# Kernel tuning notes

Hardware: AMD Instinct MI355X
Metric: run time of the kernel (lower is better)

## Reference

```python
import jax, jax.numpy as jnp
import numpy as np

B, N, D = 4, 2048, 512
H = 8            # num_heads (even)
HE = H // 2      # effective heads = 4
DH = D // H      # head_dim = 64
LAMBDA_INIT = 0.8
EPS = 1e-5


def setup_inputs() -> dict:
    key = jax.random.key(0)
    ks = jax.random.split(key, 10)
    return {
        "q": jax.random.normal(ks[0], (B, N, D), jnp.float32),
        "k": jax.random.normal(ks[1], (B, N, D), jnp.float32),
        "v": jax.random.normal(ks[2], (B, N, D), jnp.float32),
        "lambda_q1": 0.1 * jax.random.normal(ks[3], (DH,), jnp.float32),
        "lambda_k1": 0.1 * jax.random.normal(ks[4], (DH,), jnp.float32),
        "lambda_q2": 0.1 * jax.random.normal(ks[5], (DH,), jnp.float32),
        "lambda_k2": 0.1 * jax.random.normal(ks[6], (DH,), jnp.float32),
        "norm_w": jnp.ones((2 * DH,), jnp.float32),
        "out_w": 0.02 * jax.random.normal(ks[7], (D, D), jnp.float32),  # torch Linear weight [out,in]
        "out_b": jnp.zeros((D,), jnp.float32),
    }


def reference(q, k, v, lambda_q1, lambda_k1, lambda_q2, lambda_k2, norm_w, out_w, out_b):
    b, nq, d = q.shape
    nk = k.shape[1]
    # split heads: q,k -> [B, 2*HE, N, DH]; v -> [B, HE, Nk, 2*DH]
    qh = q.reshape(b, nq, 2 * HE, DH).transpose(0, 2, 1, 3) * (DH ** -0.5)
    kh = k.reshape(b, nk, 2 * HE, DH).transpose(0, 2, 1, 3)
    vh = v.reshape(b, nk, HE, 2 * DH).transpose(0, 2, 1, 3)
    scores = jnp.einsum('bhqd,bhkd->bhqk', qh, kh)          # [B, 2HE, Nq, Nk]
    probs = jax.nn.softmax(scores, axis=-1)
    probs = probs.reshape(b, HE, 2, nq, nk)
    lam = (jnp.exp(jnp.sum(lambda_q1 * lambda_k1))
           - jnp.exp(jnp.sum(lambda_q2 * lambda_k2)) + LAMBDA_INIT)
    diff = probs[:, :, 0] - lam * probs[:, :, 1]            # [B, HE, Nq, Nk]
    out = jnp.einsum('bhqk,bhkd->bhqd', diff, vh)           # [B, HE, Nq, 2*DH]
    # per-head RMSNorm over last dim (2*DH), elementwise affine
    out = out * jax.lax.rsqrt(jnp.mean(out * out, axis=-1, keepdims=True) + EPS)
    out = out * norm_w * (1.0 - LAMBDA_INIT)
    out = out.transpose(0, 2, 1, 3).reshape(b, nq, d)
    return out @ out_w.T + out_b
```

## Files before the change

### kernel.cpp

```cpp
#include <hip/hip_runtime.h>
#include <math.h>

#define BB 4
#define NN 2048
#define DD 512
#define LAMBDA_INIT 0.8f
#define EPSV 1e-5f

typedef __attribute__((ext_vector_type(8))) short bf16x8;
typedef __attribute__((ext_vector_type(4))) float f32x4;
typedef __attribute__((ext_vector_type(16))) float f32x16;
typedef unsigned short u16;
typedef __attribute__((ext_vector_type(4))) u16 u16x4;
typedef __attribute__((ext_vector_type(8))) u16 u16x8;
typedef __attribute__((ext_vector_type(4))) unsigned u32x4;

__device__ __forceinline__ u16 f2bf(float f) {
  unsigned u = __builtin_bit_cast(unsigned, f);
  u = (u + 0x7FFFu + ((u >> 16) & 1u)) >> 16;
  return (u16)u;
}

__device__ __forceinline__ void gload16(const void* g, void* l) {
  __builtin_amdgcn_global_load_lds((const __attribute__((address_space(1))) unsigned*)g,
                                   (__attribute__((address_space(3))) unsigned*)l, 16, 0, 0);
}

__device__ __forceinline__ f32x16 fz16() {
  f32x16 z;
  #pragma unroll
  for (int i = 0; i < 16; ++i) z[i] = 0.f;
  return z;
}

__device__ __forceinline__ void plswap(unsigned &a, unsigned &b) {
  asm("v_permlane32_swap_b32 %0, %1" : "+v"(a), "+v"(b));
}
__device__ __forceinline__ float xhalf_add(float x) {
  unsigned a = __builtin_bit_cast(unsigned, x), b;
  asm("v_mov_b32 %0, %1" : "=v"(b) : "v"(a));
  asm("v_permlane32_swap_b32 %0, %1" : "+v"(a), "+v"(b));
  return __builtin_bit_cast(float, a) + __builtin_bit_cast(float, b);
}

__global__ __launch_bounds__(256) void prep_kernel(
    const float* __restrict__ q, const float* __restrict__ k, const float* __restrict__ w,
    u16* __restrict__ Qb, u16* __restrict__ Kb, u16* __restrict__ Wb)
{
  const int t = threadIdx.x;
  const int bid = blockIdx.x;
  if (bid >= BB * NN) {
    const size_t idx = (size_t)(bid - BB * NN) * 256 + t;
    float4 f = *(const float4*)&w[idx * 4];
    u16x4 o = { f2bf(f.x), f2bf(f.y), f2bf(f.z), f2bf(f.w) };
    *(u16x4*)&Wb[idx * 4] = o;
    return;
  }
  const size_t row = bid;
  const int n = bid & (NN - 1);
  const int b = bid >> 11;
  if (t < 128) {
    const float s = 0.125f * 1.4426950408889634f;
    float4 f = *(const float4*)&q[row * DD + t * 4];
    u16x4 o = { f2bf(f.x * s), f2bf(f.y * s), f2bf(f.z * s), f2bf(f.w * s) };
    *(u16x4*)&Qb[row * DD + t * 4] = o;
  } else {
    const int f0 = (t - 128) * 4;
    float4 f = *(const float4*)&k[row * DD + f0];
    const int he = f0 >> 7, fi = f0 & 127;
    const int gi = fi >> 3, lo = fi & 7;
    const int gi2 = (gi & 8) | ((gi & 7) ^ (n & 7));
    u16x4 o = { f2bf(f.x), f2bf(f.y), f2bf(f.z), f2bf(f.w) };
    *(u16x4*)&Kb[((size_t)(b * 4 + he) * NN + n) * 128 + gi2 * 8 + lo] = o;
  }
}

__global__ __launch_bounds__(256) void v_prep_kernel(const float* __restrict__ v, u16* __restrict__ Vbt) {
  __shared__ u16 Ls[64][72];
  const int t = threadIdx.x;
  const int n0 = blockIdx.x * 64;
  const int d0 = blockIdx.y * 64;
  const int z  = blockIdx.z;
  #pragma unroll
  for (int p = 0; p < 4; ++p) {
    int n = p * 16 + (t >> 4), f4 = t & 15;
    float4 rv = *(const float4*)&v[((size_t)((z >> 2) * NN + n0 + n)) * DD + (z & 3) * 128 + d0 + f4 * 4];
    Ls[n][f4*4+0] = f2bf(rv.x); Ls[n][f4*4+1] = f2bf(rv.y);
    Ls[n][f4*4+2] = f2bf(rv.z); Ls[n][f4*4+3] = f2bf(rv.w);
  }
  __syncthreads();
  #pragma unroll
  for (int rep = 0; rep < 2; ++rep) {
    const int sid   = rep * 256 + t;
    const int tt    = sid >> 8;
    const int rem   = sid & 255;
    const int i_rel = rem >> 6;
    const int ls    = rem & 63;
    const int i_    = (d0 >> 4) + i_rel;
    const int j     = i_ * 8 + (ls >> 3);
    const int s0    = (ls & 7) ^ (j & 7);
    const int dl    = 2 * (i_rel * 8 + (ls >> 3)) + (s0 >> 2);
    const int nl0   = tt * 32 + (s0 & 3) * 8;
    u16x8 o;
    #pragma unroll
    for (int jj = 0; jj < 8; ++jj) o[jj] = Ls[nl0 + jj][dl];
    const int tile = blockIdx.x * 2 + tt;
    *(u16x8*)&Vbt[((size_t)z * 64 + tile) * 4096 + i_ * 512 + ls * 8] = o;
  }
}

#define ISSUE_K(dst, kv0) do { \
  _Pragma("unroll") for (int i_ = 0; i_ < 8; ++i_) \
    gload16(kgb + (((size_t)(kv0) + i_ * 4 + (l >> 4)) << 7) + ((l & 15) << 3), (dst) + i_ * 512); \
  __builtin_amdgcn_sched_barrier(0); } while (0)

#define ISSUE_V(dst, kv0) do { \
  _Pragma("unroll") for (int i_ = 0; i_ < 8; ++i_) \
    gload16(vgb + ((size_t)((kv0) >> 5)) * 4096 + i_ * 512 + l * 8, (dst) + i_ * 512); \
  __builtin_amdgcn_sched_barrier(0); } while (0)

#define WAIT_VM0 do { asm volatile("s_waitcnt vmcnt(0)" ::: "memory"); \
  __builtin_amdgcn_sched_barrier(0); } while (0)

__global__ __launch_bounds__(256, 2) void attn10_kernel(
    const u16* __restrict__ Qb, const u16* __restrict__ Kb, const u16* __restrict__ Vbt,
    const float* __restrict__ lq1, const float* __restrict__ lk1,
    const float* __restrict__ lq2, const float* __restrict__ lk2,
    const float* __restrict__ norm_w, u16* __restrict__ Xb)
{
  __shared__ __align__(16) u16 smem[32768];
  __shared__ float stats[2][2][2][32];

  u16* KB = smem;
  u16* VB = smem + 16384;

  const int tid = threadIdx.x;
  const int w   = tid >> 6;
  const int l   = tid & 63;
  const int hi  = l >> 5;
  const int q   = l & 31;
  const int kvh = w & 1;
  const int qh  = w >> 1;

  const int bid0 = blockIdx.x;
  const int bid = (bid0 & 7) * 64 + (bid0 >> 3);
  const int qt = bid & 31;
  const int he = (bid >> 5) & 3;
  const int b  = bid >> 7;
  const int q0 = qt * 64;
  const int bhe = b * 4 + he;
  const int qrow = q0 + qh * 32 + q;

  float lp1 = lq1[l] * lk1[l], lp2 = lq2[l] * lk2[l];
  #pragma unroll
  for (int off = 32; off; off >>= 1) { lp1 += __shfl_xor(lp1, off); lp2 += __shfl_xor(lp2, off); }
  const float lam = __expf(lp1) - __expf(lp2) + LAMBDA_INIT;
  asm volatile("" :: "v"(lam));

  bf16x8 qf[2][4];
  {
    const u16* qp = Qb + ((size_t)(b * NN) + qrow) * DD + he * 128 + hi * 8;
    #pragma unroll
    for (int h = 0; h < 2; ++h)
      #pragma unroll
      for (int dk = 0; dk < 4; ++dk)
        qf[h][dk] = *(const bf16x8*)(qp + h * 64 + dk * 16);
  }
  WAIT_VM0;
  #pragma unroll
  for (int h = 0; h < 2; ++h)
    #pragma unroll
    for (int dk = 0; dk < 4; ++dk)
      asm volatile("" :: "v"(qf[h][dk]));

  const u16* kgb = Kb + (size_t)bhe * NN * 128;
  const u16* vgb = Vbt + (size_t)bhe * 64 * 4096;
  const int kvb = kvh * 1024;

  if (qh == 0) ISSUE_K(&KB[kvh * 8192], kvb);
  else         ISSUE_V(&VB[kvh * 8192], kvb);

  f32x16 O[2][4];
  #pragma unroll
  for (int h = 0; h < 2; ++h)
    #pragma unroll
    for (int dt = 0; dt < 4; ++dt) O[h][dt] = fz16();
  float sl[2] = {0.f, 0.f};

  const int jq  = (q >> 1) & 7;
  const int dq1 = (q & 1) << 2;

  for (int tt = 0; tt < 32; ++tt) {
    WAIT_VM0;
    __builtin_amdgcn_s_barrier();
    __builtin_amdgcn_sched_barrier(0);

    if (tt != 31) {
      const int kvn = kvb + (tt + 1) * 32;
      const int db = (tt + 1) & 1;
      if (qh == 0) ISSUE_K(&KB[(kvh * 2 + db) * 4096], kvn);
      else         ISSUE_V(&VB[(kvh * 2 + db) * 4096], kvn);
    }

    const u16* Kcur = &KB[(kvh * 2 + (tt & 1)) * 4096];
    const u16* Vcur = &VB[(kvh * 2 + (tt & 1)) * 4096];

    f32x16 S[2];
    __builtin_amdgcn_s_setprio(1);
    #pragma unroll
    for (int h = 0; h < 2; ++h) {
      f32x16 acc = fz16();
      #pragma unroll
      for (int dk = 0; dk < 4; ++dk) {
        const int gd = h * 8 + dk * 2 + hi;
        const int g2 = (gd & 8) | ((gd & 7) ^ (q & 7));
        bf16x8 kf = *(const bf16x8*)&Kcur[q * 128 + g2 * 8];
        acc = __builtin_amdgcn_mfma_f32_32x32x16_bf16(kf, qf[h][dk], acc, 0, 0, 0);
      }
      S[h] = acc;
    }
    __builtin_amdgcn_s_setprio(0);

    bf16x8 pb[2][2];
    #pragma unroll
    for (int h = 0; h < 2; ++h) {
      #pragma unroll
      for (int r = 0; r < 16; ++r)
        S[h][r] = __builtin_amdgcn_exp2f(S[h][r]);
      float y0 = (S[h][0]  + S[h][1])  + (S[h][2]  + S[h][3]);
      float y1 = (S[h][4]  + S[h][5])  + (S[h][6]  + S[h][7]);
      float y2 = (S[h][8]  + S[h][9])  + (S[h][10] + S[h][11]);
      float y3 = (S[h][12] + S[h][13]) + (S[h][14] + S[h][15]);
      sl[h] += (y0 + y1) + (y2 + y3);

      unsigned PK[8];
      #pragma unroll
      for (int p2 = 0; p2 < 8; ++p2)
        asm("v_cvt_pk_bf16_f32 %0, %1, %2" : "=v"(PK[p2]) : "v"(S[h][2*p2]), "v"(S[h][2*p2+1]));
      #pragma unroll
      for (int kb = 0; kb < 2; ++kb) {
        unsigned w0 = PK[4*kb + 0], w2v = PK[4*kb + 2];
        unsigned w1 = PK[4*kb + 1], w3v = PK[4*kb + 3];
        plswap(w0, w2v);
        plswap(w1, w3v);
        union { u32x4 u; bf16x8 v; } cv;
        cv.u = (u32x4){ w0, w1, w2v, w3v };
        pb[h][kb] = cv.v;
      }
    }

    __builtin_amdgcn_s_setprio(1);
    #pragma unroll
    for (int kk = 0; kk < 2; ++kk)
      #pragma unroll
      for (int dt = 0; dt < 4; ++dt) {
        const int j = dt * 16 + (q >> 1);
        const int s8 = (dq1 + kk * 2 + hi) ^ jq;
        bf16x8 vf = *(const bf16x8*)&Vcur[j * 64 + s8 * 8];
        O[0][dt] = __builtin_amdgcn_mfma_f32_32x32x16_bf16(vf, pb[0][kk], O[0][dt], 0, 0, 0);
        O[1][dt] = __builtin_amdgcn_mfma_f32_32x32x16_bf16(vf, pb[1][kk], O[1][dt], 0, 0, 0);
      }
    __builtin_amdgcn_s_setprio(0);
  }

  const float slr0 = xhalf_add(sl[0]);
  const float slr1 = xhalf_add(sl[1]);
  __syncthreads();
  if (hi == 0) {
    stats[qh][kvh][0][q] = slr0;
    stats[qh][kvh][1][q] = slr1;
  }
  __syncthreads();
  float L[2];
  #pragma unroll
  for (int h = 0; h < 2; ++h)
    L[h] = stats[qh][0][h][q] + stats[qh][1][h][q];

  float* xch = (float*)smem;
  __syncthreads();
  if (kvh == 1) {
    #pragma unroll
    for (int h = 0; h < 2; ++h)
      #pragma unroll
      for (int dt = 0; dt < 4; ++dt)
        #pragma unroll
        for (int r = 0; r < 16; ++r)
          xch[qh * 8192 + ((h * 4 + dt) * 16 + r) * 64 + l] = O[h][dt][r];
  }
  __syncthreads();
  if (kvh == 0) {
    #pragma unroll
    for (int h = 0; h < 2; ++h)
      #pragma unroll
      for (int dt = 0; dt < 4; ++dt)
        #pragma unroll
        for (int r = 0; r < 16; ++r)
          O[h][dt][r] += xch[qh * 8192 + ((h * 4 + dt) * 16 + r) * 64 + l];

    const float i1 = 1.f / L[0];
    const float i2 = lam / L[1];
    float ss = 0.f;
    f32x16 od[4];
    #pragma unroll
    for (int dt = 0; dt < 4; ++dt)
      #pragma unroll
      for (int r = 0; r < 16; ++r) {
        float o = O[0][dt][r] * i1 - O[1][dt][r] * i2;
        od[dt][r] = o; ss += o * o;
      }
    ss += __shfl_xor(ss, 32);
    const float rstd = rsqrtf(ss * (1.f / 128.f) + EPSV);
    const size_t xo = ((size_t)(b * NN) + qrow) * DD + he * 128;
    #pragma unroll
    for (int dt = 0; dt < 4; ++dt)
      #pragma unroll
      for (int rq = 0; rq < 4; ++rq) {
        const int d0 = dt * 32 + rq * 8 + hi * 4;
        const float4 nw = *(const float4*)&norm_w[d0];
        u16x4 ov;
        ov[0] = f2bf(od[dt][rq*4 + 0] * rstd * nw.x * 0.2f);
        ov[1] = f2bf(od[dt][rq*4 + 1] * rstd * nw.y * 0.2f);
        ov[2] = f2bf(od[dt][rq*4 + 2] * rstd * nw.z * 0.2f);
        ov[3] = f2bf(od[dt][rq*4 + 3] * rstd * nw.w * 0.2f);
        *(u16x4*)&Xb[xo + d0] = ov;
      }
  }
}

#define PLOAD(k0) do { \
    _Pragma("unroll") for (int p_ = 0; p_ < 2; ++p_) { \
      int idx_ = p_*256 + t; int r_ = idx_ >> 3, gi_ = idx_ & 7; \
      ra[p_] = *(const u16x8*)&Xb[(size_t)(row0 + r_) * DD + (k0) + gi_*8]; \
      rb[p_] = *(const u16x8*)&Wb[(size_t)(col0 + r_) * DD + (k0) + gi_*8]; } \
  } while (0)
#define PWRITE(bi) do { \
    _Pragma("unroll") for (int p_ = 0; p_ < 2; ++p_) { \
      int idx_ = p_*256 + t; int r_ = idx_ >> 3, gi_ = idx_ & 7; \
      *(u16x8*)&As[bi][r_*64 + ((gi_ ^ (r_ & 7)) << 3)] = ra[p_]; \
      *(u16x8*)&Bs[bi][r_*64 + ((gi_ ^ (r_ & 7)) << 3)] = rb[p_]; } \
  } while (0)

__global__ __launch_bounds__(256, 2) void proj_mfma_kernel(
    const u16* __restrict__ Xb, const u16* __restrict__ Wb,
    const float* __restrict__ bias, float* __restrict__ out)
{
  __shared__ __align__(16) u16 As[2][64*64];
  __shared__ __align__(16) u16 Bs[2][64*64];
  const int t = threadIdx.x;
  const int w = t >> 6, l = t & 63, g = l >> 4, c = l & 15;
  const int wm = w >> 1, wn = w & 1;
  const int row0 = blockIdx.x * 64, col0 = blockIdx.y * 64;

  u16x8 ra[2], rb[2];
  f32x4 acc[2][2];
  #pragma unroll
  for (int i = 0; i < 2; ++i)
    #pragma unroll
    for (int j = 0; j < 2; ++j) acc[i][j] = (f32x4){0,0,0,0};
  float bj[2];
  #pragma unroll
  for (int j = 0; j < 2; ++j) bj[j] = bias[col0 + wn*32 + j*16 + c];

  PLOAD(0);
  PWRITE(0);
  __syncthreads();
  for (int s = 0; s < 8; ++s) {
    const int bi = s & 1;
    if (s < 7) PLOAD((s + 1) * 64);
    #pragma unroll
    for (int kc = 0; kc < 2; ++kc) {
      bf16x8 af[2], bfv[2];
      #pragma unroll
      for (int i = 0; i < 2; ++i) {
        int rowa = wm*32 + i*16 + c;
        af[i]  = *(const bf16x8*)&As[bi][rowa*64 + (((kc*4 + g) ^ (c & 7)) << 3)];
        int rowb = wn*32 + i*16 + c;
        bfv[i] = *(const bf16x8*)&Bs[bi][rowb*64 + (((kc*4 + g) ^ (c & 7)) << 3)];
      }
      #pragma unroll
      for (int i = 0; i < 2; ++i)
        #pragma unroll
        for (int j = 0; j < 2; ++j)
          acc[i][j] = __builtin_amdgcn_mfma_f32_16x16x32_bf16(af[i], bfv[j], acc[i][j], 0, 0, 0);
    }
    if (s < 7) PWRITE((s + 1) & 1);
    __syncthreads();
  }
  #pragma unroll
  for (int i = 0; i < 2; ++i)
    #pragma unroll
    for (int j = 0; j < 2; ++j)
      #pragma unroll
      for (int rr = 0; rr < 4; ++rr)
        out[(size_t)(row0 + wm*32 + i*16 + g*4 + rr) * DD + col0 + wn*32 + j*16 + c] = acc[i][j][rr] + bj[j];
}

extern "C" void kernel_launch(void* const* d_in, const int* in_sizes, int n_in,
                              void* d_out, int out_size, void* d_ws, size_t ws_size,
                              hipStream_t stream) {
    const float* q      = (const float*)d_in[0];
    const float* k      = (const float*)d_in[1];
    const float* v      = (const float*)d_in[2];
    const float* lq1    = (const float*)d_in[3];
    const float* lk1    = (const float*)d_in[4];
    const float* lq2    = (const float*)d_in[5];
    const float* lk2    = (const float*)d_in[6];
    const float* norm_w = (const float*)d_in[7];
    const float* out_w  = (const float*)d_in[8];
    const float* out_b  = (const float*)d_in[9];
    float* out = (float*)d_out;

    u16* Qb  = (u16*)d_ws;
    u16* Kb  = (u16*)((char*)d_ws + (8u  << 20));
    u16* Vbt = (u16*)((char*)d_ws + (16u << 20));
    u16* Wb  = (u16*)((char*)d_ws + (24u << 20));
    u16* Xb  = (u16*)((char*)d_ws + (25u << 20));

    prep_kernel<<<BB * NN + 256, 256, 0, stream>>>(q, k, out_w, Qb, Kb, Wb);
    v_prep_kernel<<<dim3(32, 2, 16), 256, 0, stream>>>(v, Vbt);
    attn10_kernel<<<512, 256, 0, stream>>>(Qb, Kb, Vbt, lq1, lk1, lq2, lk2, norm_w, Xb);
    proj_mfma_kernel<<<dim3(128, 8), 256, 0, stream>>>(Xb, Wb, out_b, out);
}
```

Measured before the change: 89.00 us.

## Double query tile per block and triple-buffer K/V loads with deeper prefetch

The attention kernel now runs 512 threads per block, each covering 128 query rows, so one K/V tile in LDS serves twice as many queries. All eight waves split the K and V global-to-LDS loads, and a three-stage ring buffer prefetches two tiles ahead, waiting only for the oldest batch via a partial vmcnt wait. This is meant to halve K/V reload traffic per query and hide load latency better. In exchange it uses more LDS and a larger block, which can lower occupancy, and the cross-wave reduction of partial outputs is serialized over two passes.

```diff
diff --git a/kernel.cpp b/kernel.cpp
--- a/kernel.cpp
+++ b/kernel.cpp
@@ -109,30 +109,29 @@
   }
 }
 
-#define ISSUE_K(dst, kv0) do { \
-  _Pragma("unroll") for (int i_ = 0; i_ < 8; ++i_) \
-    gload16(kgb + (((size_t)(kv0) + i_ * 4 + (l >> 4)) << 7) + ((l & 15) << 3), (dst) + i_ * 512); \
+#define ISSUE_K4(dst, kv0, half) do { \
+  _Pragma("unroll") for (int i_ = 0; i_ < 4; ++i_) { int ii_ = (half)*4 + i_; \
+    gload16(kgb + (((size_t)(kv0) + ii_ * 4 + (l >> 4)) << 7) + ((l & 15) << 3), (dst) + ii_ * 512); } \
   __builtin_amdgcn_sched_barrier(0); } while (0)
 
-#define ISSUE_V(dst, kv0) do { \
-  _Pragma("unroll") for (int i_ = 0; i_ < 8; ++i_) \
-    gload16(vgb + ((size_t)((kv0) >> 5)) * 4096 + i_ * 512 + l * 8, (dst) + i_ * 512); \
+#define ISSUE_V4(dst, kv0, half) do { \
+  _Pragma("unroll") for (int i_ = 0; i_ < 4; ++i_) { int ii_ = (half)*4 + i_; \
+    gload16(vgb + ((size_t)((kv0) >> 5)) * 4096 + ii_ * 512 + l * 8, (dst) + ii_ * 512); } \
   __builtin_amdgcn_sched_barrier(0); } while (0)
 
+#define WAIT_VM(n) do { asm volatile("s_waitcnt vmcnt(" #n ")" ::: "memory"); \
+  __builtin_amdgcn_sched_barrier(0); } while (0)
 #define WAIT_VM0 do { asm volatile("s_waitcnt vmcnt(0)" ::: "memory"); \
   __builtin_amdgcn_sched_barrier(0); } while (0)
 
-__global__ __launch_bounds__(256, 2) void attn10_kernel(
+__global__ __launch_bounds__(512, 2) void attn11_kernel(
     const u16* __restrict__ Qb, const u16* __restrict__ Kb, const u16* __restrict__ Vbt,
     const float* __restrict__ lq1, const float* __restrict__ lk1,
     const float* __restrict__ lq2, const float* __restrict__ lk2,
     const float* __restrict__ norm_w, u16* __restrict__ Xb)
 {
-  __shared__ __align__(16) u16 smem[32768];
-  __shared__ float stats[2][2][2][32];
-
-  u16* KB = smem;
-  u16* VB = smem + 16384;
+  __shared__ __align__(16) u16 smem[49152];
+  __shared__ float stats[4][2][2][32];
 
   const int tid = threadIdx.x;
   const int w   = tid >> 6;
@@ -142,12 +141,18 @@
   const int kvh = w & 1;
   const int qh  = w >> 1;
 
+  const bool jK   = w < 4;
+  const int  jrem = jK ? w : (w - 4);
+  const int  jkvh = jrem >> 1;
+  const int  jhalf= jrem & 1;
+  const int  jkvb = jkvh * 1024;
+
   const int bid0 = blockIdx.x;
-  const int bid = (bid0 & 7) * 64 + (bid0 >> 3);
-  const int qt = bid & 31;
-  const int he = (bid >> 5) & 3;
-  const int b  = bid >> 7;
-  const int q0 = qt * 64;
+  const int bid = (bid0 & 7) * 32 + (bid0 >> 3);
+  const int qt = bid & 15;
+  const int he = (bid >> 4) & 3;
+  const int b  = bid >> 6;
+  const int q0 = qt * 128;
   const int bhe = b * 4 + he;
   const int qrow = q0 + qh * 32 + q;
 
@@ -175,10 +180,13 @@
 
   const u16* kgb = Kb + (size_t)bhe * NN * 128;
   const u16* vgb = Vbt + (size_t)bhe * 64 * 4096;
-  const int kvb = kvh * 1024;
-
-  if (qh == 0) ISSUE_K(&KB[kvh * 8192], kvb);
-  else         ISSUE_V(&VB[kvh * 8192], kvb);
+
+  #pragma unroll
+  for (int pt = 0; pt < 2; ++pt) {
+    u16* dst = (jK ? smem : smem + 24576) + (jkvh * 3 + pt) * 4096;
+    if (jK) ISSUE_K4(dst, jkvb + pt * 32, jhalf);
+    else    ISSUE_V4(dst, jkvb + pt * 32, jhalf);
+  }
 
   f32x16 O[2][4];
   #pragma unroll
@@ -190,20 +198,21 @@
   const int jq  = (q >> 1) & 7;
   const int dq1 = (q & 1) << 2;
 
+  int scur = 0, spre = 2;
   for (int tt = 0; tt < 32; ++tt) {
-    WAIT_VM0;
+    WAIT_VM(4);
     __builtin_amdgcn_s_barrier();
     __builtin_amdgcn_sched_barrier(0);
 
-    if (tt != 31) {
-      const int kvn = kvb + (tt + 1) * 32;
-      const int db = (tt + 1) & 1;
-      if (qh == 0) ISSUE_K(&KB[(kvh * 2 + db) * 4096], kvn);
-      else         ISSUE_V(&VB[(kvh * 2 + db) * 4096], kvn);
-    }
-
-    const u16* Kcur = &KB[(kvh * 2 + (tt & 1)) * 4096];
-    const u16* Vcur = &VB[(kvh * 2 + (tt & 1)) * 4096];
+    {
+      const int nt = (tt + 2) & 31;
+      u16* dst = (jK ? smem : smem + 24576) + (jkvh * 3 + spre) * 4096;
+      if (jK) ISSUE_K4(dst, jkvb + nt * 32, jhalf);
+      else    ISSUE_V4(dst, jkvb + nt * 32, jhalf);
+    }
+
+    const u16* Kcur = smem + (kvh * 3 + scur) * 4096;
+    const u16* Vcur = smem + 24576 + (kvh * 3 + scur) * 4096;
 
     f32x16 S[2];
     __builtin_amdgcn_s_setprio(1);
@@ -261,11 +270,16 @@
         O[1][dt] = __builtin_amdgcn_mfma_f32_32x32x16_bf16(vf, pb[1][kk], O[1][dt], 0, 0, 0);
       }
     __builtin_amdgcn_s_setprio(0);
-  }
+
+    scur = (scur == 2) ? 0 : scur + 1;
+    spre = (spre == 2) ? 0 : spre + 1;
+  }
+
+  WAIT_VM0;
+  __syncthreads();
 
   const float slr0 = xhalf_add(sl[0]);
   const float slr1 = xhalf_add(sl[1]);
-  __syncthreads();
   if (hi == 0) {
     stats[qh][kvh][0][q] = slr0;
     stats[qh][kvh][1][q] = slr1;
@@ -277,26 +291,33 @@
     L[h] = stats[qh][0][h][q] + stats[qh][1][h][q];
 
   float* xch = (float*)smem;
+  #pragma unroll
+  for (int qp = 0; qp < 2; ++qp) {
+    const bool act = (qh >> 1) == qp;
+    __syncthreads();
+    if (act && kvh == 1) {
+      #pragma unroll
+      for (int h = 0; h < 2; ++h)
+        #pragma unroll
+        for (int dt = 0; dt < 4; ++dt)
+          #pragma unroll
+          for (int r = 0; r < 16; ++r)
+            xch[(qh & 1) * 8192 + ((h * 4 + dt) * 16 + r) * 64 + l] = O[h][dt][r];
+    }
+    __syncthreads();
+    if (act && kvh == 0) {
+      #pragma unroll
+      for (int h = 0; h < 2; ++h)
+        #pragma unroll
+        for (int dt = 0; dt < 4; ++dt)
+          #pragma unroll
+          for (int r = 0; r < 16; ++r)
+            O[h][dt][r] += xch[(qh & 1) * 8192 + ((h * 4 + dt) * 16 + r) * 64 + l];
+    }
+  }
   __syncthreads();
-  if (kvh == 1) {
-    #pragma unroll
-    for (int h = 0; h < 2; ++h)
-      #pragma unroll
-      for (int dt = 0; dt < 4; ++dt)
-        #pragma unroll
-        for (int r = 0; r < 16; ++r)
-          xch[qh * 8192 + ((h * 4 + dt) * 16 + r) * 64 + l] = O[h][dt][r];
-  }
-  __syncthreads();
+
   if (kvh == 0) {
-    #pragma unroll
-    for (int h = 0; h < 2; ++h)
-      #pragma unroll
-      for (int dt = 0; dt < 4; ++dt)
-        #pragma unroll
-        for (int r = 0; r < 16; ++r)
-          O[h][dt][r] += xch[qh * 8192 + ((h * 4 + dt) * 16 + r) * 64 + l];
-
     const float i1 = 1.f / L[0];
     const float i2 = lam / L[1];
     float ss = 0.f;
@@ -418,6 +439,6 @@
 
     prep_kernel<<<BB * NN + 256, 256, 0, stream>>>(q, k, out_w, Qb, Kb, Wb);
     v_prep_kernel<<<dim3(32, 2, 16), 256, 0, stream>>>(v, Vbt);
-    attn10_kernel<<<512, 256, 0, stream>>>(Qb, Kb, Vbt, lq1, lk1, lq2, lk2, norm_w, Xb);
+    attn11_kernel<<<256, 512, 0, stream>>>(Qb, Kb, Vbt, lq1, lk1, lq2, lk2, norm_w, Xb);
     proj_mfma_kernel<<<dim3(128, 8), 256, 0, stream>>>(Xb, Wb, out_b, out);
 }
```

Result: faster. 86.87 us (-2.4%).

## Software-pipeline attention loop: overlap PV of previous tile with QK and softmax

Applied to the files above, without the earlier changes.

Restructures the attention main loop so each iteration computes QK for the current KV tile, then the PV product for the previous tile's probabilities, then the exp/pack for the current tile. MFMA work can then overlap the transcendental and pack instructions instead of running strictly one after the other. V tiles go into a triple buffer because a V tile is consumed one iteration later than its K tile, so shared memory grows and the stats array moves into that buffer. The last iteration issues a redundant wrap-around prefetch, which is waited on before smem reuse.

```diff
diff --git a/kernel.cpp b/kernel.cpp
--- a/kernel.cpp
+++ b/kernel.cpp
@@ -122,14 +122,62 @@
 #define WAIT_VM0 do { asm volatile("s_waitcnt vmcnt(0)" ::: "memory"); \
   __builtin_amdgcn_sched_barrier(0); } while (0)
 
-__global__ __launch_bounds__(256, 2) void attn10_kernel(
+#define DO_QK(Kcur, S) do { \
+  __builtin_amdgcn_s_setprio(1); \
+  _Pragma("unroll") for (int h = 0; h < 2; ++h) { \
+    f32x16 acc = fz16(); \
+    _Pragma("unroll") for (int dk = 0; dk < 4; ++dk) { \
+      const int gd = h * 8 + dk * 2 + hi; \
+      const int g2 = (gd & 8) | ((gd & 7) ^ (q & 7)); \
+      bf16x8 kf = *(const bf16x8*)&(Kcur)[q * 128 + g2 * 8]; \
+      acc = __builtin_amdgcn_mfma_f32_32x32x16_bf16(kf, qf[h][dk], acc, 0, 0, 0); \
+    } \
+    S[h] = acc; \
+  } \
+  __builtin_amdgcn_s_setprio(0); } while (0)
+
+#define DO_PV(Vcur, pbX) do { \
+  __builtin_amdgcn_s_setprio(1); \
+  _Pragma("unroll") for (int kk = 0; kk < 2; ++kk) \
+    _Pragma("unroll") for (int dt = 0; dt < 4; ++dt) { \
+      const int j = dt * 16 + (q >> 1); \
+      const int s8 = (dq1 + kk * 2 + hi) ^ jq; \
+      bf16x8 vf = *(const bf16x8*)&(Vcur)[j * 64 + s8 * 8]; \
+      O[0][dt] = __builtin_amdgcn_mfma_f32_32x32x16_bf16(vf, pbX[0][kk], O[0][dt], 0, 0, 0); \
+      O[1][dt] = __builtin_amdgcn_mfma_f32_32x32x16_bf16(vf, pbX[1][kk], O[1][dt], 0, 0, 0); \
+    } \
+  __builtin_amdgcn_s_setprio(0); } while (0)
+
+#define DO_SM(S, pbX) do { \
+  _Pragma("unroll") for (int h = 0; h < 2; ++h) { \
+    _Pragma("unroll") for (int r = 0; r < 16; ++r) \
+      S[h][r] = __builtin_amdgcn_exp2f(S[h][r]); \
+    float y0 = (S[h][0]  + S[h][1])  + (S[h][2]  + S[h][3]); \
+    float y1 = (S[h][4]  + S[h][5])  + (S[h][6]  + S[h][7]); \
+    float y2 = (S[h][8]  + S[h][9])  + (S[h][10] + S[h][11]); \
+    float y3 = (S[h][12] + S[h][13]) + (S[h][14] + S[h][15]); \
+    sl[h] += (y0 + y1) + (y2 + y3); \
+    unsigned PK[8]; \
+    _Pragma("unroll") for (int p2 = 0; p2 < 8; ++p2) \
+      asm("v_cvt_pk_bf16_f32 %0, %1, %2" : "=v"(PK[p2]) : "v"(S[h][2*p2]), "v"(S[h][2*p2+1])); \
+    _Pragma("unroll") for (int kb = 0; kb < 2; ++kb) { \
+      unsigned w0 = PK[4*kb + 0], w2v = PK[4*kb + 2]; \
+      unsigned w1 = PK[4*kb + 1], w3v = PK[4*kb + 3]; \
+      plswap(w0, w2v); \
+      plswap(w1, w3v); \
+      union { u32x4 u; bf16x8 v; } cv; \
+      cv.u = (u32x4){ w0, w1, w2v, w3v }; \
+      pbX[h][kb] = cv.v; \
+    } \
+  } } while (0)
+
+__global__ __launch_bounds__(256, 2) void attn12_kernel(
     const u16* __restrict__ Qb, const u16* __restrict__ Kb, const u16* __restrict__ Vbt,
     const float* __restrict__ lq1, const float* __restrict__ lk1,
     const float* __restrict__ lq2, const float* __restrict__ lk2,
     const float* __restrict__ norm_w, u16* __restrict__ Xb)
 {
-  __shared__ __align__(16) u16 smem[32768];
-  __shared__ float stats[2][2][2][32];
+  __shared__ __align__(16) u16 smem[40960];
 
   u16* KB = smem;
   u16* VB = smem + 16384;
@@ -177,8 +225,8 @@
   const u16* vgb = Vbt + (size_t)bhe * 64 * 4096;
   const int kvb = kvh * 1024;
 
-  if (qh == 0) ISSUE_K(&KB[kvh * 8192], kvb);
-  else         ISSUE_V(&VB[kvh * 8192], kvb);
+  if (qh == 0) ISSUE_K(&KB[(kvh * 2 + 0) * 4096], kvb);
+  else         ISSUE_V(&VB[(kvh * 3 + 0) * 4096], kvb);
 
   f32x16 O[2][4];
   #pragma unroll
@@ -186,97 +234,76 @@
     #pragma unroll
     for (int dt = 0; dt < 4; ++dt) O[h][dt] = fz16();
   float sl[2] = {0.f, 0.f};
+  bf16x8 pbP[2][2];
 
   const int jq  = (q >> 1) & 7;
   const int dq1 = (q & 1) << 2;
 
-  for (int tt = 0; tt < 32; ++tt) {
+  {
     WAIT_VM0;
     __builtin_amdgcn_s_barrier();
     __builtin_amdgcn_sched_barrier(0);
-
-    if (tt != 31) {
-      const int kvn = kvb + (tt + 1) * 32;
-      const int db = (tt + 1) & 1;
-      if (qh == 0) ISSUE_K(&KB[(kvh * 2 + db) * 4096], kvn);
-      else         ISSUE_V(&VB[(kvh * 2 + db) * 4096], kvn);
+    if (qh == 0) ISSUE_K(&KB[(kvh * 2 + 1) * 4096], kvb + 32);
+    else         ISSUE_V(&VB[(kvh * 3 + 1) * 4096], kvb + 32);
+    const u16* Kcur = &KB[(kvh * 2 + 0) * 4096];
+    f32x16 S[2];
+    DO_QK(Kcur, S);
+    DO_SM(S, pbP);
+  }
+
+  int vprev = 0, vnext = 2;
+  for (int tt = 1; tt < 32; ++tt) {
+    WAIT_VM0;
+    __builtin_amdgcn_s_barrier();
+    __builtin_amdgcn_sched_barrier(0);
+
+    {
+      const int kvn = kvb + ((tt + 1) & 31) * 32;
+      if (qh == 0) ISSUE_K(&KB[(kvh * 2 + ((tt + 1) & 1)) * 4096], kvn);
+      else         ISSUE_V(&VB[(kvh * 3 + vnext) * 4096], kvn);
     }
 
-    const u16* Kcur = &KB[(kvh * 2 + (tt & 1)) * 4096];
-    const u16* Vcur = &VB[(kvh * 2 + (tt & 1)) * 4096];
+    const u16* Kcur  = &KB[(kvh * 2 + (tt & 1)) * 4096];
+    const u16* Vprev = &VB[(kvh * 3 + vprev) * 4096];
 
     f32x16 S[2];
-    __builtin_amdgcn_s_setprio(1);
-    #pragma unroll
-    for (int h = 0; h < 2; ++h) {
-      f32x16 acc = fz16();
-      #pragma unroll
-      for (int dk = 0; dk < 4; ++dk) {
-        const int gd = h * 8 + dk * 2 + hi;
-        const int g2 = (gd & 8) | ((gd & 7) ^ (q & 7));
-        bf16x8 kf = *(const bf16x8*)&Kcur[q * 128 + g2 * 8];
-        acc = __builtin_amdgcn_mfma_f32_32x32x16_bf16(kf, qf[h][dk], acc, 0, 0, 0);
-      }
-      S[h] = acc;
-    }
-    __builtin_amdgcn_s_setprio(0);
-
-    bf16x8 pb[2][2];
-    #pragma unroll
-    for (int h = 0; h < 2; ++h) {
-      #pragma unroll
-      for (int r = 0; r < 16; ++r)
-        S[h][r] = __builtin_amdgcn_exp2f(S[h][r]);
-      float y0 = (S[h][0]  + S[h][1])  + (S[h][2]  + S[h][3]);
-      float y1 = (S[h][4]  + S[h][5])  + (S[h][6]  + S[h][7]);
-      float y2 = (S[h][8]  + S[h][9])  + (S[h][10] + S[h][11]);
-      float y3 = (S[h][12] + S[h][13]) + (S[h][14] + S[h][15]);
-      sl[h] += (y0 + y1) + (y2 + y3);
-
-      unsigned PK[8];
-      #pragma unroll
-      for (int p2 = 0; p2 < 8; ++p2)
-        asm("v_cvt_pk_bf16_f32 %0, %1, %2" : "=v"(PK[p2]) : "v"(S[h][2*p2]), "v"(S[h][2*p2+1]));
-      #pragma unroll
-      for (int kb = 0; kb < 2; ++kb) {
-        unsigned w0 = PK[4*kb + 0], w2v = PK[4*kb + 2];
-        unsigned w1 = PK[4*kb + 1], w3v = PK[4*kb + 3];
-        plswap(w0, w2v);
-        plswap(w1, w3v);
-        union { u32x4 u; bf16x8 v; } cv;
-        cv.u = (u32x4){ w0, w1, w2v, w3v };
-        pb[h][kb] = cv.v;
-      }
-    }
-
-    __builtin_amdgcn_s_setprio(1);
-    #pragma unroll
-    for (int kk = 0; kk < 2; ++kk)
-      #pragma unroll
-      for (int dt = 0; dt < 4; ++dt) {
-        const int j = dt * 16 + (q >> 1);
-        const int s8 = (dq1 + kk * 2 + hi) ^ jq;
-        bf16x8 vf = *(const bf16x8*)&Vcur[j * 64 + s8 * 8];
-        O[0][dt] = __builtin_amdgcn_mfma_f32_32x32x16_bf16(vf, pb[0][kk], O[0][dt], 0, 0, 0);
-        O[1][dt] = __builtin_amdgcn_mfma_f32_32x32x16_bf16(vf, pb[1][kk], O[1][dt], 0, 0, 0);
-      }
-    __builtin_amdgcn_s_setprio(0);
-  }
+    DO_QK(Kcur, S);
+    DO_PV(Vprev, pbP);
+    bf16x8 pbN[2][2];
+    DO_SM(S, pbN);
+    #pragma unroll
+    for (int h = 0; h < 2; ++h)
+      #pragma unroll
+      for (int kb = 0; kb < 2; ++kb)
+        pbP[h][kb] = pbN[h][kb];
+
+    vprev = (vprev == 2) ? 0 : vprev + 1;
+    vnext = (vnext == 2) ? 0 : vnext + 1;
+  }
+
+  {
+    const u16* Vlast = &VB[(kvh * 3 + 1) * 4096];
+    DO_PV(Vlast, pbP);
+  }
+
+  WAIT_VM0;
+  __syncthreads();
+
+  float* xch   = (float*)smem;
+  float* stats = (float*)smem + 16384;
 
   const float slr0 = xhalf_add(sl[0]);
   const float slr1 = xhalf_add(sl[1]);
-  __syncthreads();
   if (hi == 0) {
-    stats[qh][kvh][0][q] = slr0;
-    stats[qh][kvh][1][q] = slr1;
+    stats[((qh * 2 + kvh) * 2 + 0) * 32 + q] = slr0;
+    stats[((qh * 2 + kvh) * 2 + 1) * 32 + q] = slr1;
   }
   __syncthreads();
   float L[2];
   #pragma unroll
   for (int h = 0; h < 2; ++h)
-    L[h] = stats[qh][0][h][q] + stats[qh][1][h][q];
-
-  float* xch = (float*)smem;
+    L[h] = stats[((qh * 2 + 0) * 2 + h) * 32 + q] + stats[((qh * 2 + 1) * 2 + h) * 32 + q];
+
   __syncthreads();
   if (kvh == 1) {
     #pragma unroll
@@ -418,6 +445,6 @@
 
     prep_kernel<<<BB * NN + 256, 256, 0, stream>>>(q, k, out_w, Qb, Kb, Wb);
     v_prep_kernel<<<dim3(32, 2, 16), 256, 0, stream>>>(v, Vbt);
-    attn10_kernel<<<512, 256, 0, stream>>>(Qb, Kb, Vbt, lq1, lk1, lq2, lk2, norm_w, Xb);
+    attn12_kernel<<<512, 256, 0, stream>>>(Qb, Kb, Vbt, lq1, lk1, lq2, lk2, norm_w, Xb);
     proj_mfma_kernel<<<dim3(128, 8), 256, 0, stream>>>(Xb, Wb, out_b, out);
 }
```

Measured after the change: 89.05 us. No clear change (+0.1%).
